# Kernel optimization log

Measured on AMD Instinct MI355X. Metric: run time of the kernel, lower is better.

## Reference

```python
import jax, jax.numpy as jnp
import numpy as np

H_OUT = 512
W_OUT = 512


def _leaky(x):
    return jnp.where(x >= 0, x, 0.2 * x)


def _spline(cp, out_size):
    # cp: [B, R, N] control points -> [B, R, out_size] cubic Hermite interp
    N = cp.shape[-1]
    nseg = N - 1
    eps = 1e-3
    t = jnp.linspace(eps, 1.0 - eps, out_size)
    ts = t * nseg
    seg = jnp.clip(jnp.floor(ts).astype(jnp.int32), 0, nseg - 1)
    tau = jnp.clip(ts - seg.astype(ts.dtype), 0.0, 0.9999)
    t2 = tau * tau
    t3 = t2 * tau
    h00 = 2 * t3 - 3 * t2 + 1
    h10 = t3 - 2 * t2 + tau
    h01 = -2 * t3 + 3 * t2
    h11 = t3 - t2
    # central-difference tangents, scaled by 1/num_segments
    m = jnp.concatenate([
        (cp[..., 1:2] - cp[..., 0:1]) * 0.5,
        (cp[..., 2:] - cp[..., :-2]) * 0.5,
        (cp[..., -1:] - cp[..., -2:-1]) * 0.5,
    ], axis=-1) / nseg
    seg1 = jnp.clip(seg + 1, 0, N - 1)
    pk = cp[..., seg]
    pk1 = cp[..., seg1]
    mk = m[..., seg]
    mk1 = m[..., seg1]
    return h00 * pk + h10 * mk + h01 * pk1 + h11 * mk1


def _gen(feats, w1, b1, w2, b2):
    # batched per-rank 2-layer MLP: feats [B,R,D], w1 [R,D,Hd], w2 [R,Hd,C]
    hdn = _leaky(jnp.einsum('brd,rdh->brh', feats, w1) + b1[None])
    return jnp.einsum('brh,rhc->brc', hdn, w2) + b2[None]


def setup_inputs() -> dict:
    key = jax.random.key(0)
    ks = iter(jax.random.split(key, 40))
    def rn(shape, s=0.05):
        return jax.random.normal(next(ks), shape, jnp.float32) * s
    B, D, Hd = 64, 768, 256
    Rm, Ra, CX, CY = 16, 8, 24, 24
    Rt = Rm + Ra
    inp = {
        'h': jax.random.normal(next(ks), (B, D), jnp.float32),
        'rank_emb': rn((Rt, Hd), 0.1),
        'st_w1': rn((D, 2 * Hd)), 'st_b1': jnp.zeros((2 * Hd,), jnp.float32),
        'st_w2': rn((2 * Hd, Hd)), 'st_b2': jnp.zeros((Hd,), jnp.float32),
        'rm_w1': rn((Rt, 2 * Hd, Hd)), 'rm_b1': jnp.zeros((Rt, Hd), jnp.float32),
        'rm_w2': rn((Rt, Hd, Hd)), 'rm_b2': jnp.zeros((Rt, Hd), jnp.float32),
        'mx_w1': rn((Rm, Hd, Hd)), 'mx_b1': jnp.zeros((Rm, Hd), jnp.float32),
        'mx_w2': rn((Rm, Hd, CX)), 'mx_b2': jnp.zeros((Rm, CX), jnp.float32),
        'my_w1': rn((Rm, Hd, Hd)), 'my_b1': jnp.zeros((Rm, Hd), jnp.float32),
        'my_w2': rn((Rm, Hd, CY)), 'my_b2': jnp.zeros((Rm, CY), jnp.float32),
        'ax_w1': rn((Ra, Hd, Hd)), 'ax_b1': jnp.zeros((Ra, Hd), jnp.float32),
        'ax_w2': rn((Ra, Hd, CX)), 'ax_b2': jnp.zeros((Ra, CX), jnp.float32),
        'ay_w1': rn((Ra, Hd, Hd)), 'ay_b1': jnp.zeros((Ra, Hd), jnp.float32),
        'ay_w2': rn((Ra, Hd, CY)), 'ay_b2': jnp.zeros((Ra, CY), jnp.float32),
        'mult_w': jnp.ones((Rm,), jnp.float32) / Rm,
        'addx_w': jnp.ones((Ra,), jnp.float32) / Ra * 0.5,
        'addy_w': jnp.ones((Ra,), jnp.float32) / Ra * 0.5,
        'gbias': jnp.asarray(0.5, jnp.float32),
    }
    return inp


def reference(h, rank_emb, st_w1, st_b1, st_w2, st_b2,
              rm_w1, rm_b1, rm_w2, rm_b2,
              mx_w1, mx_b1, mx_w2, mx_b2,
              my_w1, my_b1, my_w2, my_b2,
              ax_w1, ax_b1, ax_w2, ax_b2,
              ay_w1, ay_b1, ay_w2, ay_b2,
              mult_w, addx_w, addy_w, gbias):
    B = h.shape[0]
    Rt = rank_emb.shape[0]
    Rm = mx_w1.shape[0]
    # shared conditioning
    shared = _leaky(h @ st_w1 + st_b1) @ st_w2 + st_b2  # [B, Hd]
    comb = jnp.concatenate([
        jnp.broadcast_to(shared[:, None, :], (B, Rt, shared.shape[-1])),
        jnp.broadcast_to(rank_emb[None], (B, Rt, rank_emb.shape[-1])),
    ], axis=-1)  # [B, Rt, 2*Hd]
    rf = _gen(comb, rm_w1, rm_b1, rm_w2, rm_b2)  # [B, Rt, Hd]
    fm, fa = rf[:, :Rm], rf[:, Rm:]
    Px_m = _gen(fm, mx_w1, mx_b1, mx_w2, mx_b2)  # [B, Rm, CX]
    Py_m = _gen(fm, my_w1, my_b1, my_w2, my_b2)
    Px_a = _gen(fa, ax_w1, ax_b1, ax_w2, ax_b2)
    Py_a = _gen(fa, ay_w1, ay_b1, ay_w2, ay_b2)
    u = _spline(Px_m, W_OUT)   # [B, Rm, W]
    v = _spline(Py_m, H_OUT)   # [B, Rm, H]
    a_x = _spline(Px_a, W_OUT)
    b_y = _spline(Py_a, H_OUT)
    depth_mult = jnp.einsum('brw,brh,r->bhw', u, v, jax.nn.softmax(mult_w))
    dx = jnp.einsum('brw,r->bw', a_x, jax.nn.softmax(addx_w))
    dy = jnp.einsum('brh,r->bh', b_y, jax.nn.softmax(addy_w))
    depth = depth_mult + dx[:, None, :] + dy[:, :, None] + gbias
    return depth[:, None]  # [B, 1, H, W]
```

## Files before the change

kernel.cpp:

```cpp
#include <hip/hip_runtime.h>


__device__ __forceinline__ float leaky(float v) { return v >= 0.f ? v : 0.2f * v; }

__global__ __launch_bounds__(256, 2) void l1_kernel(
    const float* __restrict__ h, const float* __restrict__ W,
    const float* __restrict__ bias, float* __restrict__ outp)
{
    __shared__ __align__(16) float a_lds[128][34];
    __shared__ __align__(16) float w_lds[128][34];
    const int tid = threadIdx.x;
    const int x = blockIdx.x, z = blockIdx.z;
    const int b0 = (x & 1) * 32, n0 = (x >> 1) * 32;
    const int nq = tid & 15, bq = tid >> 4;
    const int k0 = z * 128;
    float a00, a01, a10, a11;
    if (z == 0) {
        float bv0 = bias[n0 + nq * 2], bv1 = bias[n0 + nq * 2 + 1];
        a00 = bv0; a01 = bv1; a10 = bv0; a11 = bv1;
    } else { a00 = a01 = a10 = a11 = 0.f; }
    #pragma unroll
    for (int j = 0; j < 16; ++j) {
        int idx = tid + j * 256;
        int k = idx & 127, c = idx >> 7;
        a_lds[k][c] = h[(size_t)(b0 + c) * 768 + k0 + k];
        int n = idx & 31, kk = idx >> 5;
        w_lds[kk][n] = W[(size_t)(k0 + kk) * 512 + n0 + n];
    }
    __syncthreads();
    #pragma unroll 32
    for (int kk = 0; kk < 128; ++kk) {
        float2 a = *(const float2*)&a_lds[kk][bq * 2];
        float2 w = *(const float2*)&w_lds[kk][nq * 2];
        a00 += a.x * w.x; a01 += a.x * w.y;
        a10 += a.y * w.x; a11 += a.y * w.y;
    }
    float* ob = outp + (size_t)z * 32768;
    ob[(size_t)(b0 + bq * 2) * 512 + n0 + nq * 2]         = a00;
    ob[(size_t)(b0 + bq * 2) * 512 + n0 + nq * 2 + 1]     = a01;
    ob[(size_t)(b0 + bq * 2 + 1) * 512 + n0 + nq * 2]     = a10;
    ob[(size_t)(b0 + bq * 2 + 1) * 512 + n0 + nq * 2 + 1] = a11;
}

__global__ __launch_bounds__(512, 2) void l2_kernel(
    const float* __restrict__ hid1p, const float* __restrict__ st_w2,
    const float* __restrict__ st_b2, float* __restrict__ sh)
{
    __shared__ __align__(16) float hid_s[2][512];
    __shared__ __align__(16) float ps2[2][2][256];
    const int tid = threadIdx.x;
    const int b0 = blockIdx.x * 2;
    if (tid < 256) {
        int row = tid >> 7, j4 = tid & 127;
        const float4* hp = (const float4*)hid1p;
        size_t off = (size_t)(b0 + row) * 128 + j4;
        float4 v0 = hp[off],         v1 = hp[8192 + off],  v2 = hp[16384 + off];
        float4 v3 = hp[24576 + off], v4 = hp[32768 + off], v5 = hp[40960 + off];
        float4 s;
        s.x = leaky(v0.x + v1.x + v2.x + v3.x + v4.x + v5.x);
        s.y = leaky(v0.y + v1.y + v2.y + v3.y + v4.y + v5.y);
        s.z = leaky(v0.z + v1.z + v2.z + v3.z + v4.z + v5.z);
        s.w = leaky(v0.w + v1.w + v2.w + v3.w + v4.w + v5.w);
        ((float4*)&hid_s[row][0])[j4] = s;
    }
    __syncthreads();
    {
        const int col = tid & 255, kg = tid >> 8;
        const int o = kg * 256;
        float a0 = 0.f, a1 = 0.f;
        const float* wp = st_w2 + (size_t)o * 256 + col;
        #pragma unroll 4
        for (int d = 0; d < 256; d += 4) {
            float w0 = wp[(size_t)(d + 0) * 256], w1 = wp[(size_t)(d + 1) * 256];
            float w2 = wp[(size_t)(d + 2) * 256], w3 = wp[(size_t)(d + 3) * 256];
            float4 s0 = *(const float4*)&hid_s[0][o + d];
            float4 s1 = *(const float4*)&hid_s[1][o + d];
            a0 += s0.x * w0 + s0.y * w1 + s0.z * w2 + s0.w * w3;
            a1 += s1.x * w0 + s1.y * w1 + s1.z * w2 + s1.w * w3;
        }
        ps2[kg][0][col] = a0; ps2[kg][1][col] = a1;
    }
    __syncthreads();
    {
        int row = tid >> 8, c = tid & 255;
        sh[(size_t)(b0 + row) * 256 + c] = st_b2[c] + ps2[0][row][c] + ps2[1][row][c];
    }
}

__global__ __launch_bounds__(512, 4) void mega_kernel(
    const float* __restrict__ sh,
    const float* __restrict__ rank_emb,
    const float* __restrict__ rm_w1, const float* __restrict__ rm_b1,
    const float* __restrict__ rm_w2, const float* __restrict__ rm_b2,
    const float* __restrict__ mx_w1, const float* __restrict__ mx_b1,
    const float* __restrict__ mx_w2, const float* __restrict__ mx_b2,
    const float* __restrict__ my_w1, const float* __restrict__ my_b1,
    const float* __restrict__ my_w2, const float* __restrict__ my_b2,
    const float* __restrict__ ax_w1, const float* __restrict__ ax_b1,
    const float* __restrict__ ax_w2, const float* __restrict__ ax_b2,
    const float* __restrict__ ay_w1, const float* __restrict__ ay_b1,
    const float* __restrict__ ay_w2, const float* __restrict__ ay_b2,
    float* __restrict__ Pcat)
{
    __shared__ __align__(16) float sh_s[4][256];
    __shared__ __align__(16) float hdn_s[4][256];
    __shared__ __align__(16) float rf_s[4][256];
    __shared__ __align__(16) float hc_s[2][4][256];
    __shared__ __align__(16) float re_ps[2][256];
    __shared__ __align__(16) float remb_s[256];
    const int tid = threadIdx.x;
    const int blk = blockIdx.x;
    const int r = blk % 24;
    const int bt = blk / 24;
    const int b0 = bt * 4;
    const int col = tid & 255, rh = tid >> 8;
    const int r0 = rh * 2;

    if (tid < 256) {
        ((float4*)sh_s)[tid] = ((const float4*)sh)[(size_t)b0 * 64 + tid];
    } else if (tid < 320) {
        int j4 = tid - 256;
        ((float4*)remb_s)[j4] = ((const float4*)rank_emb)[(size_t)r * 64 + j4];
    }
    __syncthreads();

    {
        float accp = 0.f;
        const float* wb = rm_w1 + ((size_t)r * 512 + 256 + rh * 128) * 256 + col;
        const int o = rh * 128;
        #pragma unroll 4
        for (int d = 0; d < 128; d += 4) {
            float w0 = wb[(size_t)(d + 0) * 256], w1 = wb[(size_t)(d + 1) * 256];
            float w2 = wb[(size_t)(d + 2) * 256], w3 = wb[(size_t)(d + 3) * 256];
            float4 e = *(const float4*)&remb_s[o + d];
            accp += e.x * w0 + e.y * w1 + e.z * w2 + e.w * w3;
        }
        re_ps[rh][col] = accp;
    }
    __syncthreads();

    {
        float bv = rm_b1[r * 256 + col] + re_ps[0][col] + re_ps[1][col];
        float a0 = bv, a1 = bv;
        const float* wp = rm_w1 + (size_t)r * 512 * 256 + col;
        #pragma unroll 4
        for (int d = 0; d < 256; d += 4) {
            float w0 = wp[(size_t)(d + 0) * 256], w1 = wp[(size_t)(d + 1) * 256];
            float w2 = wp[(size_t)(d + 2) * 256], w3 = wp[(size_t)(d + 3) * 256];
            float4 s0 = *(const float4*)&sh_s[r0 + 0][d];
            float4 s1 = *(const float4*)&sh_s[r0 + 1][d];
            a0 += s0.x * w0 + s0.y * w1 + s0.z * w2 + s0.w * w3;
            a1 += s1.x * w0 + s1.y * w1 + s1.z * w2 + s1.w * w3;
        }
        hdn_s[r0 + 0][col] = leaky(a0); hdn_s[r0 + 1][col] = leaky(a1);
    }
    __syncthreads();

    {
        float bv = rm_b2[r * 256 + col];
        float a0 = bv, a1 = bv;
        const float* wp = rm_w2 + (size_t)r * 65536 + col;
        #pragma unroll 4
        for (int d = 0; d < 256; d += 4) {
            float w0 = wp[(size_t)(d + 0) * 256], w1 = wp[(size_t)(d + 1) * 256];
            float w2 = wp[(size_t)(d + 2) * 256], w3 = wp[(size_t)(d + 3) * 256];
            float4 s0 = *(const float4*)&hdn_s[r0 + 0][d];
            float4 s1 = *(const float4*)&hdn_s[r0 + 1][d];
            a0 += s0.x * w0 + s0.y * w1 + s0.z * w2 + s0.w * w3;
            a1 += s1.x * w0 + s1.y * w1 + s1.z * w2 + s1.w * w3;
        }
        rf_s[r0 + 0][col] = a0; rf_s[r0 + 1][col] = a1;
    }
    __syncthreads();

    const float *W1, *B1, *W2, *B2; int y;
    if (r < 16) {
        if (rh == 0) { y = r;      W1 = mx_w1 + (size_t)r * 65536;  B1 = mx_b1 + r * 256;  W2 = mx_w2 + (size_t)r * 6144;  B2 = mx_b2 + r * 24; }
        else         { y = 16 + r; W1 = my_w1 + (size_t)r * 65536;  B1 = my_b1 + r * 256;  W2 = my_w2 + (size_t)r * 6144;  B2 = my_b2 + r * 24; }
    } else {
        int rw = r - 16;
        if (rh == 0) { y = 32 + rw; W1 = ax_w1 + (size_t)rw * 65536; B1 = ax_b1 + rw * 256; W2 = ax_w2 + (size_t)rw * 6144; B2 = ax_b2 + rw * 24; }
        else         { y = 40 + rw; W1 = ay_w1 + (size_t)rw * 65536; B1 = ay_b1 + rw * 256; W2 = ay_w2 + (size_t)rw * 6144; B2 = ay_b2 + rw * 24; }
    }

    {
        float bv = B1[col];
        float acc[4];
        #pragma unroll
        for (int i = 0; i < 4; ++i) acc[i] = bv;
        const float* wp = W1 + col;
        #pragma unroll 4
        for (int d = 0; d < 256; d += 4) {
            float w0 = wp[(size_t)(d + 0) * 256], w1 = wp[(size_t)(d + 1) * 256];
            float w2 = wp[(size_t)(d + 2) * 256], w3 = wp[(size_t)(d + 3) * 256];
            #pragma unroll
            for (int i = 0; i < 4; ++i) {
                float4 s = *(const float4*)&rf_s[i][d];
                acc[i] += s.x * w0 + s.y * w1 + s.z * w2 + s.w * w3;
            }
        }
        #pragma unroll
        for (int i = 0; i < 4; ++i) hc_s[rh][i][col] = leaky(acc[i]);
    }
    __syncthreads();

    if (col < 96) {
        int row = col / 24, cj = col - row * 24;
        float acc = B2[cj];
        const float* wp = W2 + cj;
        #pragma unroll 4
        for (int d = 0; d < 256; d += 4) {
            float w0 = wp[(size_t)(d + 0) * 24], w1 = wp[(size_t)(d + 1) * 24];
            float w2 = wp[(size_t)(d + 2) * 24], w3 = wp[(size_t)(d + 3) * 24];
            float4 s = *(const float4*)&hc_s[rh][row][d];
            acc += s.x * w0 + s.y * w1 + s.z * w2 + s.w * w3;
        }
        Pcat[(size_t)(b0 + row) * 1152 + y * 24 + cj] = acc;
    }
}

__global__ __launch_bounds__(256, 2) void depth_fused_kernel(
    const float* __restrict__ Pcat,
    const float* __restrict__ mult_w, const float* __restrict__ addx_w,
    const float* __restrict__ addy_w, const float* __restrict__ gbias,
    float* __restrict__ out)
{
    __shared__ float cp[48][25];
    __shared__ float sw[33];
    __shared__ __align__(16) float u_s[16][132];
    __shared__ __align__(16) float v_s[16][132];
    __shared__ float dx_s[128], dy_s[128];
    const int tid = threadIdx.x;
    const int b = blockIdx.z, h0 = blockIdx.y * 128, w0 = blockIdx.x * 128;
    for (int idx = tid; idx < 1152; idx += 256)
        cp[idx / 24][idx % 24] = Pcat[(size_t)b * 1152 + idx];
    if (tid == 0) {
        float e[16], m, s;
        m = -1e30f; for (int i = 0; i < 16; ++i) m = fmaxf(m, mult_w[i]);
        s = 0.f;    for (int i = 0; i < 16; ++i) { e[i] = __expf(mult_w[i] - m); s += e[i]; }
        for (int i = 0; i < 16; ++i) sw[i] = e[i] / s;
        m = -1e30f; for (int i = 0; i < 8; ++i) m = fmaxf(m, addx_w[i]);
        s = 0.f;    for (int i = 0; i < 8; ++i) { e[i] = __expf(addx_w[i] - m); s += e[i]; }
        for (int i = 0; i < 8; ++i) sw[16 + i] = e[i] / s;
        m = -1e30f; for (int i = 0; i < 8; ++i) m = fmaxf(m, addy_w[i]);
        s = 0.f;    for (int i = 0; i < 8; ++i) { e[i] = __expf(addy_w[i] - m); s += e[i]; }
        for (int i = 0; i < 8; ++i) sw[24 + i] = e[i] / s;
        sw[32] = gbias[0];
    }
    __syncthreads();
    {
        const int local = tid & 127;
        const int gpos = (tid < 128 ? w0 : h0) + local;
        const float eps = 0.001f;
        float t = eps + (float)gpos * ((1.f - 2.f * eps) / 511.f);
        float ts = t * 23.f;
        int seg = (int)ts; if (seg > 22) seg = 22;
        float tau = ts - (float)seg;
        tau = fminf(fmaxf(tau, 0.f), 0.9999f);
        float t2 = tau * tau, t3 = t2 * tau;
        float h00 = 2.f * t3 - 3.f * t2 + 1.f;
        float h10 = t3 - 2.f * t2 + tau;
        float h01 = -2.f * t3 + 3.f * t2;
        float h11 = t3 - t2;
        int sm1 = seg > 0 ? seg - 1 : 0;
        int s1 = seg + 1;
        int sp2 = s1 < 23 ? s1 + 1 : 23;
        const float msc = 0.5f / 23.f;
        auto spl = [&](int row) -> float {
            float pk = cp[row][seg], pk1 = cp[row][s1];
            float mk  = msc * (pk1 - cp[row][sm1]);
            float mk1 = msc * (cp[row][sp2] - pk);
            return h00 * pk + h10 * mk + h01 * pk1 + h11 * mk1;
        };
        if (tid < 128) {
            #pragma unroll
            for (int r = 0; r < 16; ++r) u_s[r][local] = sw[r] * spl(r);
            float dx = sw[32];
            #pragma unroll
            for (int r = 0; r < 8; ++r) dx += sw[16 + r] * spl(32 + r);
            dx_s[local] = dx;
        } else {
            #pragma unroll
            for (int r = 0; r < 16; ++r) v_s[r][local] = spl(16 + r);
            float dy = 0.f;
            #pragma unroll
            for (int r = 0; r < 8; ++r) dy += sw[24 + r] * spl(40 + r);
            dy_s[local] = dy;
        }
    }
    __syncthreads();
    const int tw = tid & 15, th = tid >> 4;
    float acc[8][8];
    #pragma unroll
    for (int i = 0; i < 8; ++i)
        #pragma unroll
        for (int j = 0; j < 8; ++j) acc[i][j] = 0.f;
    #pragma unroll
    for (int r = 0; r < 16; ++r) {
        float4 va0 = *(const float4*)&v_s[r][th * 8];
        float4 va1 = *(const float4*)&v_s[r][th * 8 + 4];
        float4 ub0 = *(const float4*)&u_s[r][tw * 8];
        float4 ub1 = *(const float4*)&u_s[r][tw * 8 + 4];
        float va[8] = {va0.x, va0.y, va0.z, va0.w, va1.x, va1.y, va1.z, va1.w};
        float ub[8] = {ub0.x, ub0.y, ub0.z, ub0.w, ub1.x, ub1.y, ub1.z, ub1.w};
        #pragma unroll
        for (int i = 0; i < 8; ++i)
            #pragma unroll
            for (int j = 0; j < 8; ++j)
                acc[i][j] += va[i] * ub[j];
    }
    #pragma unroll
    for (int i = 0; i < 8; ++i) {
        float dyh = dy_s[th * 8 + i];
        float* op = out + (size_t)b * 262144 + (size_t)(h0 + th * 8 + i) * 512 + w0 + tw * 8;
        float4 o0, o1;
        o0.x = acc[i][0] + dx_s[tw * 8 + 0] + dyh;
        o0.y = acc[i][1] + dx_s[tw * 8 + 1] + dyh;
        o0.z = acc[i][2] + dx_s[tw * 8 + 2] + dyh;
        o0.w = acc[i][3] + dx_s[tw * 8 + 3] + dyh;
        o1.x = acc[i][4] + dx_s[tw * 8 + 4] + dyh;
        o1.y = acc[i][5] + dx_s[tw * 8 + 5] + dyh;
        o1.z = acc[i][6] + dx_s[tw * 8 + 6] + dyh;
        o1.w = acc[i][7] + dx_s[tw * 8 + 7] + dyh;
        *(float4*)op = o0;
        *(float4*)(op + 4) = o1;
    }
}

extern "C" void kernel_launch(void* const* d_in, const int* in_sizes, int n_in,
                              void* d_out, int out_size, void* d_ws, size_t ws_size,
                              hipStream_t stream) {
    const float* in_h     = (const float*)d_in[0];
    const float* rank_emb = (const float*)d_in[1];
    const float* st_w1    = (const float*)d_in[2];
    const float* st_b1    = (const float*)d_in[3];
    const float* st_w2    = (const float*)d_in[4];
    const float* st_b2    = (const float*)d_in[5];
    const float* rm_w1    = (const float*)d_in[6];
    const float* rm_b1    = (const float*)d_in[7];
    const float* rm_w2    = (const float*)d_in[8];
    const float* rm_b2    = (const float*)d_in[9];
    const float* mx_w1    = (const float*)d_in[10];
    const float* mx_b1    = (const float*)d_in[11];
    const float* mx_w2    = (const float*)d_in[12];
    const float* mx_b2    = (const float*)d_in[13];
    const float* my_w1    = (const float*)d_in[14];
    const float* my_b1    = (const float*)d_in[15];
    const float* my_w2    = (const float*)d_in[16];
    const float* my_b2    = (const float*)d_in[17];
    const float* ax_w1    = (const float*)d_in[18];
    const float* ax_b1    = (const float*)d_in[19];
    const float* ax_w2    = (const float*)d_in[20];
    const float* ax_b2    = (const float*)d_in[21];
    const float* ay_w1    = (const float*)d_in[22];
    const float* ay_b1    = (const float*)d_in[23];
    const float* ay_w2    = (const float*)d_in[24];
    const float* ay_b2    = (const float*)d_in[25];
    const float* mult_w   = (const float*)d_in[26];
    const float* addx_w   = (const float*)d_in[27];
    const float* addy_w   = (const float*)d_in[28];
    const float* gbias    = (const float*)d_in[29];
    (void)in_sizes; (void)n_in; (void)out_size; (void)ws_size;

    float* ws = (float*)d_ws;
    float* hid1p = ws;
    float* Pcat  = ws + 196608;
    float* shbuf = ws + 270336;

    l1_kernel<<<dim3(32, 1, 6), 256, 0, stream>>>(in_h, st_w1, st_b1, hid1p);

    l2_kernel<<<32, 512, 0, stream>>>(hid1p, st_w2, st_b2, shbuf);

    mega_kernel<<<384, 512, 0, stream>>>(
        shbuf, rank_emb,
        rm_w1, rm_b1, rm_w2, rm_b2,
        mx_w1, mx_b1, mx_w2, mx_b2,
        my_w1, my_b1, my_w2, my_b2,
        ax_w1, ax_b1, ax_w2, ax_b2,
        ay_w1, ay_b1, ay_w2, ay_b2,
        Pcat);

    depth_fused_kernel<<<dim3(4, 4, 64), 256, 0, stream>>>(
        Pcat, mult_w, addx_w, addy_w, gbias, (float*)d_out);
}
```

Measured before the change: 240.1 us.

## Hoist rank-embedding projection into l2 kernel and halve batch per mega block

The batch-independent rank_emb @ rm_w1 projection moves out of mega_kernel into extra blocks of the l2 kernel, so it is computed once per rank rather than once per batch tile. mega_kernel now handles 2 batch rows per block instead of 4, doubling the grid to 768 blocks. It splits the K dimension of the rm layers across the two half-blocks and splits the final small GEMV across 4 K-quarters with an LDS reduction. The aim is more parallelism and less redundant work. In exchange, each mx/my/ax/ay/rm weight is read by twice as many blocks, and extra syncs are added.

```diff
diff --git a/kernel.cpp b/kernel.cpp
--- a/kernel.cpp
+++ b/kernel.cpp
@@ -42,55 +42,83 @@
     ob[(size_t)(b0 + bq * 2 + 1) * 512 + n0 + nq * 2 + 1] = a11;
 }
 
-__global__ __launch_bounds__(512, 2) void l2_kernel(
+__global__ __launch_bounds__(512, 2) void l2re_kernel(
     const float* __restrict__ hid1p, const float* __restrict__ st_w2,
-    const float* __restrict__ st_b2, float* __restrict__ sh)
+    const float* __restrict__ st_b2,
+    const float* __restrict__ rank_emb,
+    const float* __restrict__ rm_w1, const float* __restrict__ rm_b1,
+    float* __restrict__ sh, float* __restrict__ re)
 {
     __shared__ __align__(16) float hid_s[2][512];
     __shared__ __align__(16) float ps2[2][2][256];
+    __shared__ __align__(16) float remb_s[256];
     const int tid = threadIdx.x;
-    const int b0 = blockIdx.x * 2;
-    if (tid < 256) {
-        int row = tid >> 7, j4 = tid & 127;
-        const float4* hp = (const float4*)hid1p;
-        size_t off = (size_t)(b0 + row) * 128 + j4;
-        float4 v0 = hp[off],         v1 = hp[8192 + off],  v2 = hp[16384 + off];
-        float4 v3 = hp[24576 + off], v4 = hp[32768 + off], v5 = hp[40960 + off];
-        float4 s;
-        s.x = leaky(v0.x + v1.x + v2.x + v3.x + v4.x + v5.x);
-        s.y = leaky(v0.y + v1.y + v2.y + v3.y + v4.y + v5.y);
-        s.z = leaky(v0.z + v1.z + v2.z + v3.z + v4.z + v5.z);
-        s.w = leaky(v0.w + v1.w + v2.w + v3.w + v4.w + v5.w);
-        ((float4*)&hid_s[row][0])[j4] = s;
-    }
-    __syncthreads();
-    {
-        const int col = tid & 255, kg = tid >> 8;
-        const int o = kg * 256;
-        float a0 = 0.f, a1 = 0.f;
-        const float* wp = st_w2 + (size_t)o * 256 + col;
-        #pragma unroll 4
-        for (int d = 0; d < 256; d += 4) {
-            float w0 = wp[(size_t)(d + 0) * 256], w1 = wp[(size_t)(d + 1) * 256];
-            float w2 = wp[(size_t)(d + 2) * 256], w3 = wp[(size_t)(d + 3) * 256];
-            float4 s0 = *(const float4*)&hid_s[0][o + d];
-            float4 s1 = *(const float4*)&hid_s[1][o + d];
-            a0 += s0.x * w0 + s0.y * w1 + s0.z * w2 + s0.w * w3;
-            a1 += s1.x * w0 + s1.y * w1 + s1.z * w2 + s1.w * w3;
-        }
-        ps2[kg][0][col] = a0; ps2[kg][1][col] = a1;
-    }
-    __syncthreads();
-    {
-        int row = tid >> 8, c = tid & 255;
-        sh[(size_t)(b0 + row) * 256 + c] = st_b2[c] + ps2[0][row][c] + ps2[1][row][c];
+    if (blockIdx.x < 32) {
+        const int b0 = blockIdx.x * 2;
+        if (tid < 256) {
+            int row = tid >> 7, j4 = tid & 127;
+            const float4* hp = (const float4*)hid1p;
+            size_t off = (size_t)(b0 + row) * 128 + j4;
+            float4 v0 = hp[off],         v1 = hp[8192 + off],  v2 = hp[16384 + off];
+            float4 v3 = hp[24576 + off], v4 = hp[32768 + off], v5 = hp[40960 + off];
+            float4 s;
+            s.x = leaky(v0.x + v1.x + v2.x + v3.x + v4.x + v5.x);
+            s.y = leaky(v0.y + v1.y + v2.y + v3.y + v4.y + v5.y);
+            s.z = leaky(v0.z + v1.z + v2.z + v3.z + v4.z + v5.z);
+            s.w = leaky(v0.w + v1.w + v2.w + v3.w + v4.w + v5.w);
+            ((float4*)&hid_s[row][0])[j4] = s;
+        }
+        __syncthreads();
+        {
+            const int col = tid & 255, kg = tid >> 8;
+            const int o = kg * 256;
+            float a0 = 0.f, a1 = 0.f;
+            const float* wp = st_w2 + (size_t)o * 256 + col;
+            #pragma unroll 4
+            for (int d = 0; d < 256; d += 4) {
+                float w0 = wp[(size_t)(d + 0) * 256], w1 = wp[(size_t)(d + 1) * 256];
+                float w2 = wp[(size_t)(d + 2) * 256], w3 = wp[(size_t)(d + 3) * 256];
+                float4 s0 = *(const float4*)&hid_s[0][o + d];
+                float4 s1 = *(const float4*)&hid_s[1][o + d];
+                a0 += s0.x * w0 + s0.y * w1 + s0.z * w2 + s0.w * w3;
+                a1 += s1.x * w0 + s1.y * w1 + s1.z * w2 + s1.w * w3;
+            }
+            ps2[kg][0][col] = a0; ps2[kg][1][col] = a1;
+        }
+        __syncthreads();
+        {
+            int row = tid >> 8, c = tid & 255;
+            sh[(size_t)(b0 + row) * 256 + c] = st_b2[c] + ps2[0][row][c] + ps2[1][row][c];
+        }
+    } else {
+        const int r = blockIdx.x - 32;
+        if (tid < 64)
+            ((float4*)remb_s)[tid] = ((const float4*)rank_emb)[(size_t)r * 64 + tid];
+        __syncthreads();
+        {
+            const int col = tid & 255, kh = tid >> 8;
+            const int o = kh * 128;
+            float acc = 0.f;
+            const float* wb = rm_w1 + ((size_t)r * 512 + 256 + o) * 256 + col;
+            #pragma unroll 8
+            for (int d = 0; d < 128; d += 4) {
+                float w0 = wb[(size_t)(d + 0) * 256], w1 = wb[(size_t)(d + 1) * 256];
+                float w2 = wb[(size_t)(d + 2) * 256], w3 = wb[(size_t)(d + 3) * 256];
+                float4 e = *(const float4*)&remb_s[o + d];
+                acc += e.x * w0 + e.y * w1 + e.z * w2 + e.w * w3;
+            }
+            ps2[kh][0][col] = acc;
+        }
+        __syncthreads();
+        if (tid < 256)
+            re[(size_t)r * 256 + tid] = rm_b1[r * 256 + tid] + ps2[0][0][tid] + ps2[1][0][tid];
     }
 }
 
 __global__ __launch_bounds__(512, 4) void mega_kernel(
     const float* __restrict__ sh,
-    const float* __restrict__ rank_emb,
-    const float* __restrict__ rm_w1, const float* __restrict__ rm_b1,
+    const float* __restrict__ re,
+    const float* __restrict__ rm_w1,
     const float* __restrict__ rm_w2, const float* __restrict__ rm_b2,
     const float* __restrict__ mx_w1, const float* __restrict__ mx_b1,
     const float* __restrict__ mx_w2, const float* __restrict__ mx_b2,
@@ -102,120 +130,118 @@
     const float* __restrict__ ay_w2, const float* __restrict__ ay_b2,
     float* __restrict__ Pcat)
 {
-    __shared__ __align__(16) float sh_s[4][256];
-    __shared__ __align__(16) float hdn_s[4][256];
-    __shared__ __align__(16) float rf_s[4][256];
-    __shared__ __align__(16) float hc_s[2][4][256];
-    __shared__ __align__(16) float re_ps[2][256];
-    __shared__ __align__(16) float remb_s[256];
+    __shared__ __align__(16) float sh_s[2][256];
+    __shared__ __align__(16) float hdn_s[2][256];
+    __shared__ __align__(16) float rf_s[2][256];
+    __shared__ __align__(16) float hc_s[2][2][256];
+    __shared__ __align__(16) float ps[2][2][256];
     const int tid = threadIdx.x;
     const int blk = blockIdx.x;
     const int r = blk % 24;
     const int bt = blk / 24;
-    const int b0 = bt * 4;
+    const int b0 = bt * 2;
     const int col = tid & 255, rh = tid >> 8;
-    const int r0 = rh * 2;
-
-    if (tid < 256) {
+
+    if (tid < 128)
         ((float4*)sh_s)[tid] = ((const float4*)sh)[(size_t)b0 * 64 + tid];
-    } else if (tid < 320) {
-        int j4 = tid - 256;
-        ((float4*)remb_s)[j4] = ((const float4*)rank_emb)[(size_t)r * 64 + j4];
-    }
     __syncthreads();
 
     {
-        float accp = 0.f;
-        const float* wb = rm_w1 + ((size_t)r * 512 + 256 + rh * 128) * 256 + col;
+        float a0 = 0.f, a1 = 0.f;
         const int o = rh * 128;
-        #pragma unroll 4
+        const float* wp = rm_w1 + ((size_t)r * 512 + o) * 256 + col;
+        #pragma unroll 8
         for (int d = 0; d < 128; d += 4) {
-            float w0 = wb[(size_t)(d + 0) * 256], w1 = wb[(size_t)(d + 1) * 256];
-            float w2 = wb[(size_t)(d + 2) * 256], w3 = wb[(size_t)(d + 3) * 256];
-            float4 e = *(const float4*)&remb_s[o + d];
-            accp += e.x * w0 + e.y * w1 + e.z * w2 + e.w * w3;
-        }
-        re_ps[rh][col] = accp;
-    }
+            float w0 = wp[(size_t)(d + 0) * 256], w1 = wp[(size_t)(d + 1) * 256];
+            float w2 = wp[(size_t)(d + 2) * 256], w3 = wp[(size_t)(d + 3) * 256];
+            float4 s0 = *(const float4*)&sh_s[0][o + d];
+            float4 s1 = *(const float4*)&sh_s[1][o + d];
+            a0 += s0.x * w0 + s0.y * w1 + s0.z * w2 + s0.w * w3;
+            a1 += s1.x * w0 + s1.y * w1 + s1.z * w2 + s1.w * w3;
+        }
+        ps[rh][0][col] = a0; ps[rh][1][col] = a1;
+    }
+    __syncthreads();
+    hdn_s[rh][col] = leaky(re[(size_t)r * 256 + col] + ps[0][rh][col] + ps[1][rh][col]);
     __syncthreads();
 
     {
-        float bv = rm_b1[r * 256 + col] + re_ps[0][col] + re_ps[1][col];
+        float a0 = 0.f, a1 = 0.f;
+        const int o = rh * 128;
+        const float* wp = rm_w2 + (size_t)r * 65536 + (size_t)o * 256 + col;
+        #pragma unroll 8
+        for (int d = 0; d < 128; d += 4) {
+            float w0 = wp[(size_t)(d + 0) * 256], w1 = wp[(size_t)(d + 1) * 256];
+            float w2 = wp[(size_t)(d + 2) * 256], w3 = wp[(size_t)(d + 3) * 256];
+            float4 s0 = *(const float4*)&hdn_s[0][o + d];
+            float4 s1 = *(const float4*)&hdn_s[1][o + d];
+            a0 += s0.x * w0 + s0.y * w1 + s0.z * w2 + s0.w * w3;
+            a1 += s1.x * w0 + s1.y * w1 + s1.z * w2 + s1.w * w3;
+        }
+        ps[rh][0][col] = a0; ps[rh][1][col] = a1;
+    }
+    __syncthreads();
+    rf_s[rh][col] = rm_b2[r * 256 + col] + ps[0][rh][col] + ps[1][rh][col];
+    __syncthreads();
+
+    const float *W1, *B1, *W2_0, *B2_0, *W2_1, *B2_1; int y0, y1;
+    if (r < 16) {
+        y0 = r;       y1 = 16 + r;
+        W2_0 = mx_w2 + (size_t)r * 6144;  B2_0 = mx_b2 + r * 24;
+        W2_1 = my_w2 + (size_t)r * 6144;  B2_1 = my_b2 + r * 24;
+        W1 = (rh == 0) ? mx_w1 + (size_t)r * 65536 : my_w1 + (size_t)r * 65536;
+        B1 = (rh == 0) ? mx_b1 + r * 256           : my_b1 + r * 256;
+    } else {
+        int rw = r - 16;
+        y0 = 32 + rw;  y1 = 40 + rw;
+        W2_0 = ax_w2 + (size_t)rw * 6144; B2_0 = ax_b2 + rw * 24;
+        W2_1 = ay_w2 + (size_t)rw * 6144; B2_1 = ay_b2 + rw * 24;
+        W1 = (rh == 0) ? ax_w1 + (size_t)rw * 65536 : ay_w1 + (size_t)rw * 65536;
+        B1 = (rh == 0) ? ax_b1 + rw * 256           : ay_b1 + rw * 256;
+    }
+
+    {
+        float bv = B1[col];
         float a0 = bv, a1 = bv;
-        const float* wp = rm_w1 + (size_t)r * 512 * 256 + col;
-        #pragma unroll 4
+        const float* wp = W1 + col;
+        #pragma unroll 8
         for (int d = 0; d < 256; d += 4) {
             float w0 = wp[(size_t)(d + 0) * 256], w1 = wp[(size_t)(d + 1) * 256];
             float w2 = wp[(size_t)(d + 2) * 256], w3 = wp[(size_t)(d + 3) * 256];
-            float4 s0 = *(const float4*)&sh_s[r0 + 0][d];
-            float4 s1 = *(const float4*)&sh_s[r0 + 1][d];
+            float4 s0 = *(const float4*)&rf_s[0][d];
+            float4 s1 = *(const float4*)&rf_s[1][d];
             a0 += s0.x * w0 + s0.y * w1 + s0.z * w2 + s0.w * w3;
             a1 += s1.x * w0 + s1.y * w1 + s1.z * w2 + s1.w * w3;
         }
-        hdn_s[r0 + 0][col] = leaky(a0); hdn_s[r0 + 1][col] = leaky(a1);
-    }
-    __syncthreads();
-
-    {
-        float bv = rm_b2[r * 256 + col];
-        float a0 = bv, a1 = bv;
-        const float* wp = rm_w2 + (size_t)r * 65536 + col;
-        #pragma unroll 4
-        for (int d = 0; d < 256; d += 4) {
-            float w0 = wp[(size_t)(d + 0) * 256], w1 = wp[(size_t)(d + 1) * 256];
-            float w2 = wp[(size_t)(d + 2) * 256], w3 = wp[(size_t)(d + 3) * 256];
-            float4 s0 = *(const float4*)&hdn_s[r0 + 0][d];
-            float4 s1 = *(const float4*)&hdn_s[r0 + 1][d];
-            a0 += s0.x * w0 + s0.y * w1 + s0.z * w2 + s0.w * w3;
-            a1 += s1.x * w0 + s1.y * w1 + s1.z * w2 + s1.w * w3;
-        }
-        rf_s[r0 + 0][col] = a0; rf_s[r0 + 1][col] = a1;
-    }
-    __syncthreads();
-
-    const float *W1, *B1, *W2, *B2; int y;
-    if (r < 16) {
-        if (rh == 0) { y = r;      W1 = mx_w1 + (size_t)r * 65536;  B1 = mx_b1 + r * 256;  W2 = mx_w2 + (size_t)r * 6144;  B2 = mx_b2 + r * 24; }
-        else         { y = 16 + r; W1 = my_w1 + (size_t)r * 65536;  B1 = my_b1 + r * 256;  W2 = my_w2 + (size_t)r * 6144;  B2 = my_b2 + r * 24; }
-    } else {
-        int rw = r - 16;
-        if (rh == 0) { y = 32 + rw; W1 = ax_w1 + (size_t)rw * 65536; B1 = ax_b1 + rw * 256; W2 = ax_w2 + (size_t)rw * 6144; B2 = ax_b2 + rw * 24; }
-        else         { y = 40 + rw; W1 = ay_w1 + (size_t)rw * 65536; B1 = ay_b1 + rw * 256; W2 = ay_w2 + (size_t)rw * 6144; B2 = ay_b2 + rw * 24; }
-    }
-
-    {
-        float bv = B1[col];
-        float acc[4];
-        #pragma unroll
-        for (int i = 0; i < 4; ++i) acc[i] = bv;
-        const float* wp = W1 + col;
-        #pragma unroll 4
-        for (int d = 0; d < 256; d += 4) {
-            float w0 = wp[(size_t)(d + 0) * 256], w1 = wp[(size_t)(d + 1) * 256];
-            float w2 = wp[(size_t)(d + 2) * 256], w3 = wp[(size_t)(d + 3) * 256];
-            #pragma unroll
-            for (int i = 0; i < 4; ++i) {
-                float4 s = *(const float4*)&rf_s[i][d];
-                acc[i] += s.x * w0 + s.y * w1 + s.z * w2 + s.w * w3;
-            }
-        }
-        #pragma unroll
-        for (int i = 0; i < 4; ++i) hc_s[rh][i][col] = leaky(acc[i]);
-    }
-    __syncthreads();
-
-    if (col < 96) {
-        int row = col / 24, cj = col - row * 24;
-        float acc = B2[cj];
-        const float* wp = W2 + cj;
-        #pragma unroll 4
-        for (int d = 0; d < 256; d += 4) {
-            float w0 = wp[(size_t)(d + 0) * 24], w1 = wp[(size_t)(d + 1) * 24];
-            float w2 = wp[(size_t)(d + 2) * 24], w3 = wp[(size_t)(d + 3) * 24];
-            float4 s = *(const float4*)&hc_s[rh][row][d];
+        hc_s[rh][0][col] = leaky(a0); hc_s[rh][1][col] = leaky(a1);
+    }
+    __syncthreads();
+
+    float* psf = &ps[0][0][0];
+    if (tid < 384) {
+        int o = tid >> 2, kq = tid & 3;
+        int h = o / 48, rc = o % 48;
+        int row = rc / 24, cj = rc - row * 24;
+        const float* wp = (h ? W2_1 : W2_0) + (size_t)(kq * 64) * 24 + cj;
+        const float* hp = &hc_s[h][row][kq * 64];
+        float acc = 0.f;
+        #pragma unroll 8
+        for (int d = 0; d < 64; d += 4) {
+            float w0 = wp[(d + 0) * 24], w1 = wp[(d + 1) * 24];
+            float w2 = wp[(d + 2) * 24], w3 = wp[(d + 3) * 24];
+            float4 s = *(const float4*)&hp[d];
             acc += s.x * w0 + s.y * w1 + s.z * w2 + s.w * w3;
         }
-        Pcat[(size_t)(b0 + row) * 1152 + y * 24 + cj] = acc;
+        psf[tid] = acc;
+    }
+    __syncthreads();
+    if (tid < 96) {
+        int h = tid / 48, rc = tid - h * 48;
+        int row = rc / 24, cj = rc - row * 24;
+        float v = (h ? B2_1 : B2_0)[cj]
+                + psf[tid * 4] + psf[tid * 4 + 1] + psf[tid * 4 + 2] + psf[tid * 4 + 3];
+        int y = h ? y1 : y0;
+        Pcat[(size_t)(b0 + row) * 1152 + y * 24 + cj] = v;
     }
 }
 
@@ -366,14 +392,16 @@
     float* hid1p = ws;
     float* Pcat  = ws + 196608;
     float* shbuf = ws + 270336;
+    float* rebuf = ws + 286720;
 
     l1_kernel<<<dim3(32, 1, 6), 256, 0, stream>>>(in_h, st_w1, st_b1, hid1p);
 
-    l2_kernel<<<32, 512, 0, stream>>>(hid1p, st_w2, st_b2, shbuf);
-
-    mega_kernel<<<384, 512, 0, stream>>>(
-        shbuf, rank_emb,
-        rm_w1, rm_b1, rm_w2, rm_b2,
+    l2re_kernel<<<56, 512, 0, stream>>>(hid1p, st_w2, st_b2,
+                                        rank_emb, rm_w1, rm_b1, shbuf, rebuf);
+
+    mega_kernel<<<768, 512, 0, stream>>>(
+        shbuf, rebuf,
+        rm_w1, rm_w2, rm_b2,
         mx_w1, mx_b1, mx_w2, mx_b2,
         my_w1, my_b1, my_w2, my_b2,
         ax_w1, ax_b1, ax_w2, ax_b2,
```

Result: slower. 246.8 us (+2.8%).
